# Optimization experiments

Measured on AMD Instinct MI355X. Metric: run time of the kernel, lower is better.

## Reference

```python
import jax, jax.numpy as jnp
import numpy as np

NUM_HEADS = 8
Q_DIM = 32  # == k_dim == v_dim (required by the broadcasted matmul in the source)

def _conv1x1(x, w, b):
    # x: [B, C, H, W]; w: [O, C]; b: [O]  (1x1 conv == channel matmul)
    return jnp.einsum('bchw,oc->bohw', x, w) + b[None, :, None, None]

def setup_inputs() -> dict:
    key = jax.random.key(0)
    ks = jax.random.split(key, 7)
    B, C, H, W = 16, 256, 64, 64
    O = Q_DIM * NUM_HEADS  # 256
    s = 1.0 / np.sqrt(C)
    return {
        'x':  jax.random.normal(ks[0], (B, C, H, W), jnp.float32),
        'wq': jax.random.normal(ks[1], (O, C), jnp.float32) * s,
        'bq': jax.random.normal(ks[2], (O,), jnp.float32) * 0.01,
        'wk': jax.random.normal(ks[3], (O, C), jnp.float32) * s,
        'bk': jax.random.normal(ks[4], (O,), jnp.float32) * 0.01,
        'wv': jax.random.normal(ks[5], (O, C), jnp.float32) * s,
        'bv': jax.random.normal(ks[6], (O,), jnp.float32) * 0.01,
    }

def reference(x, wq, bq, wk, bk, wv, bv):
    B, C, H, W = x.shape
    nH, d = NUM_HEADS, Q_DIM
    q = _conv1x1(x, wq, bq).reshape(B, nH, d, H, W)
    k = _conv1x1(x, wk, bk).reshape(B, nH, d, H, W)
    v = _conv1x1(x, wv, bv).reshape(B, nH, d, H, W)
    # torch.matmul(q, k.transpose(-2,-1)): contract over width, batched over (B, nH, d)
    scores = jnp.einsum('bndhw,bndgw->bndhg', q, k) / jnp.sqrt(jnp.asarray(d, x.dtype))
    weights = jax.nn.softmax(scores, axis=-1)  # [B, nH, d, H, H]
    ctx = jnp.einsum('bndhg,bndgw->bndhw', weights, v)
    return ctx.reshape(B, nH * d, H, W)
```

## Files before the change

kernel.cpp:

```cpp
#include <hip/hip_runtime.h>
#include <stdint.h>

#define LOG2E       1.4426950408889634f
#define INV_SQRT32  0.17677669529663687f

using bf16x8 = __attribute__((ext_vector_type(8))) short;
using f32x4  = __attribute__((ext_vector_type(4))) float;

__device__ __forceinline__ unsigned short f2bf(float f) {
  union { float f; uint32_t u; } v; v.f = f;
  uint32_t r = v.u + 0x7fffu + ((v.u >> 16) & 1u);
  return (unsigned short)(r >> 16);
}

typedef const __attribute__((address_space(1))) void* gas_ptr;
typedef __attribute__((address_space(3))) void*       las_ptr;
__device__ __forceinline__ void load_lds16(const void* g, void* l) {
  __builtin_amdgcn_global_load_lds((gas_ptr)g, (las_ptr)l, 16, 0, 0);
}

__global__ __launch_bounds__(256) void convert_w(
    const float* __restrict__ wq, const float* __restrict__ bq,
    const float* __restrict__ wk, const float* __restrict__ bk,
    const float* __restrict__ wv, const float* __restrict__ bv,
    unsigned short* __restrict__ Wcat, float* __restrict__ biasc) {
  int idx = (blockIdx.x * 256 + threadIdx.x) * 4;
  int p = idx >> 16;
  int rem = idx & 0xffff;
  const float* src = (p == 0) ? wq : (p == 1) ? wk : wv;
  float4 v = *(const float4*)(src + rem);
  ushort4 o;
  o.x = f2bf(v.x); o.y = f2bf(v.y); o.z = f2bf(v.z); o.w = f2bf(v.w);
  *(ushort4*)(Wcat + idx) = o;
  if (blockIdx.x < 3) {
    const float* sb = (blockIdx.x == 0) ? bq : (blockIdx.x == 1) ? bk : bv;
    biasc[blockIdx.x * 256 + threadIdx.x] = sb[threadIdx.x];
  }
}

__global__ __launch_bounds__(256) void transpose_x(const float* __restrict__ x,
                                                   unsigned short* __restrict__ xt) {
  __shared__ float tile[64 * 65];
  int b = blockIdx.z;
  int s0 = blockIdx.x * 64, c0 = blockIdx.y * 64;
  int t = threadIdx.x;
  int sl = t & 63, g = t >> 6;
  const float* xp = x + ((size_t)(b * 256 + c0)) * 4096 + s0 + sl;
#pragma unroll
  for (int ii = 0; ii < 16; ++ii) {
    int cl = g * 16 + ii;
    tile[cl * 65 + sl] = xp[(size_t)cl * 4096];
  }
  __syncthreads();
  int c8 = (t & 7) * 8;
  int rbase = t >> 3;
#pragma unroll
  for (int half = 0; half < 2; ++half) {
    int row = rbase + half * 32;
    unsigned short p[8];
#pragma unroll
    for (int i = 0; i < 8; ++i) p[i] = f2bf(tile[(c8 + i) * 65 + row]);
    *(uint4*)&xt[((size_t)(b * 4096 + s0 + row)) * 256 + c0 + c8] = *(uint4*)p;
  }
}

__global__ __launch_bounds__(256) void gemm_qkv(
    const unsigned short* __restrict__ Wc, const float* __restrict__ biasc,
    const unsigned short* __restrict__ Xt, unsigned short* __restrict__ qkv) {
  __shared__ unsigned short As[8 * 64 * 32];
  __shared__ unsigned short Bs[8 * 64 * 32];
  int nt = blockIdx.x, mt = blockIdx.y, b = blockIdx.z;
  int m0 = mt * 64, n0 = nt * 64;
  int t = threadIdx.x;
  int lane = t & 63, wave = t >> 6;
  int lr = lane >> 2;
  int lk = (lane & 3) * 8;
  const unsigned short* Abase = Wc + (size_t)m0 * 256;
  const unsigned short* Bbase = Xt + ((size_t)b * 4096 + n0) * 256;

#pragma unroll
  for (int r4 = 0; r4 < 4; ++r4) {
#pragma unroll
    for (int cc = 0; cc < 2; ++cc) {
      int kc = wave * 2 + cc;
      load_lds16(Abase + (size_t)(r4 * 16 + lr) * 256 + kc * 32 + lk,
                 &As[kc * 2048 + r4 * 512]);
      load_lds16(Bbase + (size_t)(r4 * 16 + lr) * 256 + kc * 32 + lk,
                 &Bs[kc * 2048 + r4 * 512]);
    }
  }
  __syncthreads();

  int rt = lane & 15, quad = lane >> 4;
  int wm = wave >> 1, wn = wave & 1;
  f32x4 acc[2][2];
#pragma unroll
  for (int i = 0; i < 2; ++i)
#pragma unroll
    for (int j = 0; j < 2; ++j) acc[i][j] = (f32x4){0.f, 0.f, 0.f, 0.f};

#pragma unroll
  for (int kc = 0; kc < 8; ++kc) {
    bf16x8 a0 = *(const bf16x8*)&As[kc * 2048 + (wm * 32 + rt) * 32 + quad * 8];
    bf16x8 a1 = *(const bf16x8*)&As[kc * 2048 + (wm * 32 + 16 + rt) * 32 + quad * 8];
    bf16x8 b0 = *(const bf16x8*)&Bs[kc * 2048 + (wn * 32 + rt) * 32 + quad * 8];
    bf16x8 b1 = *(const bf16x8*)&Bs[kc * 2048 + (wn * 32 + 16 + rt) * 32 + quad * 8];
    acc[0][0] = __builtin_amdgcn_mfma_f32_16x16x32_bf16(a0, b0, acc[0][0], 0, 0, 0);
    acc[0][1] = __builtin_amdgcn_mfma_f32_16x16x32_bf16(a0, b1, acc[0][1], 0, 0, 0);
    acc[1][0] = __builtin_amdgcn_mfma_f32_16x16x32_bf16(a1, b0, acc[1][0], 0, 0, 0);
    acc[1][1] = __builtin_amdgcn_mfma_f32_16x16x32_bf16(a1, b1, acc[1][1], 0, 0, 0);
  }

  size_t obase = (size_t)b * 768;
#pragma unroll
  for (int mi = 0; mi < 2; ++mi) {
    int orow = m0 + wm * 32 + mi * 16 + quad * 4;
#pragma unroll
    for (int r = 0; r < 4; ++r) {
      float bv = biasc[orow + r];
#pragma unroll
      for (int ni = 0; ni < 2; ++ni) {
        int s = n0 + wn * 32 + ni * 16 + rt;
        qkv[(obase + orow + r) * 4096 + s] = f2bf(acc[mi][ni][r] + bv);
      }
    }
  }
}

__global__ __launch_bounds__(256) void attn(const unsigned short* __restrict__ qkv,
                                            float* __restrict__ out) {
  __shared__ char sh[36608];
  unsigned short* Qs = (unsigned short*)sh;
  unsigned short* Ks = (unsigned short*)(sh + 9216);
  float*          Sf = (float*)sh;
  unsigned short* Ps = (unsigned short*)(sh + 16640);
  unsigned short* Vt = (unsigned short*)(sh + 25856);
  float* red    = (float*)(sh + 35072);
  float* rowmax = (float*)(sh + 36096);
  float* rowinv = (float*)(sh + 36352);

  int blk = blockIdx.x;
  int b = blk >> 8, o = blk & 255;
  int t = threadIdx.x;
  size_t base = ((size_t)b * 768 + o) * 4096;
  const unsigned short* qg = qkv + base;
  const unsigned short* kg = qkv + base + (size_t)256 * 4096;
  const unsigned short* vg = qkv + base + (size_t)512 * 4096;

  {
    int h = t >> 2, w0 = (t & 3) * 16;
    const uint4* qp = (const uint4*)(qg + h * 64 + w0);
    const uint4* kp = (const uint4*)(kg + h * 64 + w0);
    uint4 q0 = qp[0], q1 = qp[1];
    uint4 k0 = kp[0], k1 = kp[1];
    *(uint4*)&Qs[h * 72 + w0]     = q0;
    *(uint4*)&Qs[h * 72 + w0 + 8] = q1;
    *(uint4*)&Ks[h * 72 + w0]     = k0;
    *(uint4*)&Ks[h * 72 + w0 + 8] = k1;

    int w = t & 63, gb = (t >> 6) * 16;
    unsigned short vv[16];
#pragma unroll
    for (int j = 0; j < 16; ++j) vv[j] = vg[(size_t)(gb + j) * 64 + w];
    *(uint4*)&Vt[w * 72 + gb]     = ((uint4*)vv)[0];
    *(uint4*)&Vt[w * 72 + gb + 8] = ((uint4*)vv)[1];
  }
  __syncthreads();

  int lane = t & 63, wave = t >> 6;
  int rt = lane & 15, quad = lane >> 4;
  int wm = wave >> 1, wn = wave & 1;

  f32x4 accs[2][2];
#pragma unroll
  for (int i = 0; i < 2; ++i)
#pragma unroll
    for (int j = 0; j < 2; ++j) accs[i][j] = (f32x4){0.f, 0.f, 0.f, 0.f};
#pragma unroll
  for (int ks = 0; ks < 2; ++ks) {
    int kk = ks * 32 + quad * 8;
    bf16x8 a0 = *(const bf16x8*)&Qs[(wm * 32 + rt) * 72 + kk];
    bf16x8 a1 = *(const bf16x8*)&Qs[(wm * 32 + 16 + rt) * 72 + kk];
    bf16x8 b0 = *(const bf16x8*)&Ks[(wn * 32 + rt) * 72 + kk];
    bf16x8 b1 = *(const bf16x8*)&Ks[(wn * 32 + 16 + rt) * 72 + kk];
    accs[0][0] = __builtin_amdgcn_mfma_f32_16x16x32_bf16(a0, b0, accs[0][0], 0, 0, 0);
    accs[0][1] = __builtin_amdgcn_mfma_f32_16x16x32_bf16(a0, b1, accs[0][1], 0, 0, 0);
    accs[1][0] = __builtin_amdgcn_mfma_f32_16x16x32_bf16(a1, b0, accs[1][0], 0, 0, 0);
    accs[1][1] = __builtin_amdgcn_mfma_f32_16x16x32_bf16(a1, b1, accs[1][1], 0, 0, 0);
  }
  __syncthreads();

#pragma unroll
  for (int tm = 0; tm < 2; ++tm)
#pragma unroll
    for (int tn = 0; tn < 2; ++tn)
#pragma unroll
      for (int r = 0; r < 4; ++r)
        Sf[(wm * 32 + tm * 16 + quad * 4 + r) * 65 + wn * 32 + tn * 16 + rt] =
            accs[tm][tn][r] * INV_SQRT32;
  __syncthreads();

  int hr = t & 63, qt = t >> 6;
  float s[16];
#pragma unroll
  for (int e = 0; e < 16; ++e) s[e] = Sf[hr * 65 + qt * 16 + e];
  float m = s[0];
#pragma unroll
  for (int e = 1; e < 16; ++e) m = fmaxf(m, s[e]);
  red[qt * 64 + hr] = m;
  __syncthreads();
  if (t < 64)
    rowmax[t] = fmaxf(fmaxf(red[t], red[64 + t]), fmaxf(red[128 + t], red[192 + t]));
  __syncthreads();
  float mr = rowmax[hr];
  float ssum = 0.f;
  unsigned short pv[16];
#pragma unroll
  for (int e = 0; e < 16; ++e) {
    float p = exp2f((s[e] - mr) * LOG2E);
    ssum += p;
    pv[e] = f2bf(p);
  }
  *(uint4*)&Ps[hr * 72 + qt * 16]     = ((uint4*)pv)[0];
  *(uint4*)&Ps[hr * 72 + qt * 16 + 8] = ((uint4*)pv)[1];
  red[qt * 64 + hr] = ssum;
  __syncthreads();
  if (t < 64) rowinv[t] = 1.f / (red[t] + red[64 + t] + red[128 + t] + red[192 + t]);
  __syncthreads();

  f32x4 acco[2][2];
#pragma unroll
  for (int i = 0; i < 2; ++i)
#pragma unroll
    for (int j = 0; j < 2; ++j) acco[i][j] = (f32x4){0.f, 0.f, 0.f, 0.f};
#pragma unroll
  for (int ks = 0; ks < 2; ++ks) {
    int kk = ks * 32 + quad * 8;
    bf16x8 a0 = *(const bf16x8*)&Ps[(wm * 32 + rt) * 72 + kk];
    bf16x8 a1 = *(const bf16x8*)&Ps[(wm * 32 + 16 + rt) * 72 + kk];
    bf16x8 b0 = *(const bf16x8*)&Vt[(wn * 32 + rt) * 72 + kk];
    bf16x8 b1 = *(const bf16x8*)&Vt[(wn * 32 + 16 + rt) * 72 + kk];
    acco[0][0] = __builtin_amdgcn_mfma_f32_16x16x32_bf16(a0, b0, acco[0][0], 0, 0, 0);
    acco[0][1] = __builtin_amdgcn_mfma_f32_16x16x32_bf16(a0, b1, acco[0][1], 0, 0, 0);
    acco[1][0] = __builtin_amdgcn_mfma_f32_16x16x32_bf16(a1, b0, acco[1][0], 0, 0, 0);
    acco[1][1] = __builtin_amdgcn_mfma_f32_16x16x32_bf16(a1, b1, acco[1][1], 0, 0, 0);
  }

  float* op = out + ((size_t)(b * 256 + o)) * 4096;
#pragma unroll
  for (int tm = 0; tm < 2; ++tm) {
#pragma unroll
    for (int r = 0; r < 4; ++r) {
      int h = wm * 32 + tm * 16 + quad * 4 + r;
      float inv = rowinv[h];
#pragma unroll
      for (int tn = 0; tn < 2; ++tn) {
        int w = wn * 32 + tn * 16 + rt;
        op[h * 64 + w] = acco[tm][tn][r] * inv;
      }
    }
  }
}

extern "C" void kernel_launch(void* const* d_in, const int* in_sizes, int n_in,
                              void* d_out, int out_size, void* d_ws, size_t ws_size,
                              hipStream_t stream) {
  const float* x  = (const float*)d_in[0];
  const float* wq = (const float*)d_in[1];
  const float* bq = (const float*)d_in[2];
  const float* wk = (const float*)d_in[3];
  const float* bk = (const float*)d_in[4];
  const float* wv = (const float*)d_in[5];
  const float* bv = (const float*)d_in[6];
  float* out = (float*)d_out;

  char* ws = (char*)d_ws;
  unsigned short* Wcat  = (unsigned short*)ws;
  float*          biasc = (float*)(ws + 393216);
  unsigned short* Xt    = (unsigned short*)(ws + 396288);
  unsigned short* qkv   = (unsigned short*)(ws + 396288 + 33554432);

  hipLaunchKernelGGL(convert_w, dim3(192), dim3(256), 0, stream,
                     wq, bq, wk, bk, wv, bv, Wcat, biasc);
  hipLaunchKernelGGL(transpose_x, dim3(64, 4, 16), dim3(256), 0, stream, x, Xt);
  hipLaunchKernelGGL(gemm_qkv, dim3(64, 12, 16), dim3(256), 0, stream, Wcat, biasc, Xt, qkv);
  hipLaunchKernelGGL(attn, dim3(4096), dim3(256), 0, stream, qkv, out);
}
```

Measured before the change: 213.5 us.

## Enlarge QKV GEMM tiles to 128x256 with K-loop staging

The QKV projection GEMM moves from 64x64 output tiles, which loaded the full K=256 into LDS at once, to 128x256 tiles that walk K in four 64-wide chunks. Each wave now computes a 64x128 sub-tile with 32 MFMA accumulators, so every loaded A/B fragment is reused across more MFMAs and global/LDS traffic per FLOP drops. The grid shrinks from 12288 to 1536 blocks. In exchange, register use and accumulator pressure rise sharply, which can cut occupancy. The K-chunk loads are also not double-buffered, so load latency is exposed at each chunk.

```diff
diff --git a/kernel.cpp b/kernel.cpp
--- a/kernel.cpp
+++ b/kernel.cpp
@@ -67,10 +67,10 @@
 __global__ __launch_bounds__(256) void gemm_qkv(
     const unsigned short* __restrict__ Wc, const float* __restrict__ biasc,
     const unsigned short* __restrict__ Xt, unsigned short* __restrict__ qkv) {
-  __shared__ unsigned short As[8 * 64 * 32];
-  __shared__ unsigned short Bs[8 * 64 * 32];
+  __shared__ unsigned short As[2 * 128 * 32];
+  __shared__ unsigned short Bs[2 * 256 * 32];
   int nt = blockIdx.x, mt = blockIdx.y, b = blockIdx.z;
-  int m0 = mt * 64, n0 = nt * 64;
+  int m0 = mt * 128, n0 = nt * 256;
   int t = threadIdx.x;
   int lane = t & 63, wave = t >> 6;
   int lr = lane >> 2;
@@ -78,51 +78,60 @@
   const unsigned short* Abase = Wc + (size_t)m0 * 256;
   const unsigned short* Bbase = Xt + ((size_t)b * 4096 + n0) * 256;
 
-#pragma unroll
-  for (int r4 = 0; r4 < 4; ++r4) {
-#pragma unroll
-    for (int cc = 0; cc < 2; ++cc) {
-      int kc = wave * 2 + cc;
-      load_lds16(Abase + (size_t)(r4 * 16 + lr) * 256 + kc * 32 + lk,
-                 &As[kc * 2048 + r4 * 512]);
-      load_lds16(Bbase + (size_t)(r4 * 16 + lr) * 256 + kc * 32 + lk,
-                 &Bs[kc * 2048 + r4 * 512]);
-    }
-  }
-  __syncthreads();
-
   int rt = lane & 15, quad = lane >> 4;
   int wm = wave >> 1, wn = wave & 1;
-  f32x4 acc[2][2];
-#pragma unroll
-  for (int i = 0; i < 2; ++i)
-#pragma unroll
-    for (int j = 0; j < 2; ++j) acc[i][j] = (f32x4){0.f, 0.f, 0.f, 0.f};
-
-#pragma unroll
-  for (int kc = 0; kc < 8; ++kc) {
-    bf16x8 a0 = *(const bf16x8*)&As[kc * 2048 + (wm * 32 + rt) * 32 + quad * 8];
-    bf16x8 a1 = *(const bf16x8*)&As[kc * 2048 + (wm * 32 + 16 + rt) * 32 + quad * 8];
-    bf16x8 b0 = *(const bf16x8*)&Bs[kc * 2048 + (wn * 32 + rt) * 32 + quad * 8];
-    bf16x8 b1 = *(const bf16x8*)&Bs[kc * 2048 + (wn * 32 + 16 + rt) * 32 + quad * 8];
-    acc[0][0] = __builtin_amdgcn_mfma_f32_16x16x32_bf16(a0, b0, acc[0][0], 0, 0, 0);
-    acc[0][1] = __builtin_amdgcn_mfma_f32_16x16x32_bf16(a0, b1, acc[0][1], 0, 0, 0);
-    acc[1][0] = __builtin_amdgcn_mfma_f32_16x16x32_bf16(a1, b0, acc[1][0], 0, 0, 0);
-    acc[1][1] = __builtin_amdgcn_mfma_f32_16x16x32_bf16(a1, b1, acc[1][1], 0, 0, 0);
+
+  f32x4 acc[4][8];
+#pragma unroll
+  for (int i = 0; i < 4; ++i)
+#pragma unroll
+    for (int j = 0; j < 8; ++j) acc[i][j] = (f32x4){0.f, 0.f, 0.f, 0.f};
+
+  for (int iter = 0; iter < 4; ++iter) {
+    int k0 = iter * 64;
+    for (int i = wave; i < 48; i += 4) {
+      if (i < 16) {
+        int rb = i >> 1, kcL = i & 1;
+        load_lds16(Abase + (size_t)(rb * 16 + lr) * 256 + k0 + kcL * 32 + lk,
+                   &As[kcL * 4096 + rb * 512]);
+      } else {
+        int j = i - 16;
+        int rb = j >> 1, kcL = j & 1;
+        load_lds16(Bbase + (size_t)(rb * 16 + lr) * 256 + k0 + kcL * 32 + lk,
+                   &Bs[kcL * 8192 + rb * 512]);
+      }
+    }
+    __syncthreads();
+
+#pragma unroll
+    for (int ks = 0; ks < 2; ++ks) {
+      bf16x8 a[4];
+#pragma unroll
+      for (int mi = 0; mi < 4; ++mi)
+        a[mi] = *(const bf16x8*)&As[ks * 4096 + (wm * 64 + mi * 16 + rt) * 32 + quad * 8];
+#pragma unroll
+      for (int ni = 0; ni < 8; ++ni) {
+        bf16x8 bb = *(const bf16x8*)&Bs[ks * 8192 + (wn * 128 + ni * 16 + rt) * 32 + quad * 8];
+        acc[0][ni] = __builtin_amdgcn_mfma_f32_16x16x32_bf16(a[0], bb, acc[0][ni], 0, 0, 0);
+        acc[1][ni] = __builtin_amdgcn_mfma_f32_16x16x32_bf16(a[1], bb, acc[1][ni], 0, 0, 0);
+        acc[2][ni] = __builtin_amdgcn_mfma_f32_16x16x32_bf16(a[2], bb, acc[2][ni], 0, 0, 0);
+        acc[3][ni] = __builtin_amdgcn_mfma_f32_16x16x32_bf16(a[3], bb, acc[3][ni], 0, 0, 0);
+      }
+    }
+    __syncthreads();
   }
 
   size_t obase = (size_t)b * 768;
 #pragma unroll
-  for (int mi = 0; mi < 2; ++mi) {
-    int orow = m0 + wm * 32 + mi * 16 + quad * 4;
+  for (int mi = 0; mi < 4; ++mi) {
+    int orow = m0 + wm * 64 + mi * 16 + quad * 4;
 #pragma unroll
     for (int r = 0; r < 4; ++r) {
       float bv = biasc[orow + r];
-#pragma unroll
-      for (int ni = 0; ni < 2; ++ni) {
-        int s = n0 + wn * 32 + ni * 16 + rt;
-        qkv[(obase + orow + r) * 4096 + s] = f2bf(acc[mi][ni][r] + bv);
-      }
+      unsigned short* dst = qkv + (obase + orow + r) * 4096 + n0 + wn * 128 + rt;
+#pragma unroll
+      for (int ni = 0; ni < 8; ++ni)
+        dst[ni * 16] = f2bf(acc[mi][ni][r] + bv);
     }
   }
 }
@@ -283,6 +292,6 @@
   hipLaunchKernelGGL(convert_w, dim3(192), dim3(256), 0, stream,
                      wq, bq, wk, bk, wv, bv, Wcat, biasc);
   hipLaunchKernelGGL(transpose_x, dim3(64, 4, 16), dim3(256), 0, stream, x, Xt);
-  hipLaunchKernelGGL(gemm_qkv, dim3(64, 12, 16), dim3(256), 0, stream, Wcat, biasc, Xt, qkv);
+  hipLaunchKernelGGL(gemm_qkv, dim3(16, 6, 16), dim3(256), 0, stream, Wcat, biasc, Xt, qkv);
   hipLaunchKernelGGL(attn, dim3(4096), dim3(256), 0, stream, qkv, out);
 }
```

Result: slower. 229.3 us (+7.4%).
